# Kernel tuning notes

Measured on AMD Instinct MI355X. Metric: run time of the kernel, lower is better.

## Reference

```python
import jax, jax.numpy as jnp
import numpy as np

D_MODEL = 1024
NUM_HEADS = 16
DEPTH = D_MODEL // NUM_HEADS  # 64
BATCH = 2
SEQ = 2048


def setup_inputs() -> dict:
    key = jax.random.key(0)
    ks = jax.random.split(key, 11)
    s = 0.02
    return {
        "q": jax.random.normal(ks[0], (BATCH, SEQ, D_MODEL), dtype=jnp.float32),
        "k": jax.random.normal(ks[1], (BATCH, SEQ, D_MODEL), dtype=jnp.float32),
        "v": jax.random.normal(ks[2], (BATCH, SEQ, D_MODEL), dtype=jnp.float32),
        "wq": jax.random.normal(ks[3], (D_MODEL, D_MODEL), dtype=jnp.float32) * s,
        "bq": jnp.zeros((D_MODEL,), dtype=jnp.float32),
        "wk": jax.random.normal(ks[4], (D_MODEL, D_MODEL), dtype=jnp.float32) * s,
        "bk": jnp.zeros((D_MODEL,), dtype=jnp.float32),
        "wv": jax.random.normal(ks[5], (D_MODEL, D_MODEL), dtype=jnp.float32) * s,
        "bv": jnp.zeros((D_MODEL,), dtype=jnp.float32),
        "wo": jax.random.normal(ks[6], (D_MODEL, D_MODEL), dtype=jnp.float32) * s,
        "bo": jnp.zeros((D_MODEL,), dtype=jnp.float32),
    }


def reference(q, k, v, wq, bq, wk, bk, wv, bv, wo, bo):
    B = q.shape[0]
    # QKV projections, then split heads: (B, S, H, D)
    qh = (q @ wq + bq).reshape(B, -1, NUM_HEADS, DEPTH)
    kh = (k @ wk + bk).reshape(B, -1, NUM_HEADS, DEPTH)
    vh = (v @ wv + bv).reshape(B, -1, NUM_HEADS, DEPTH)

    inv_sqrt_dk = 1.0 / jnp.sqrt(jnp.float32(DEPTH))
    # scores: (B, Lq, Lk, H)
    scores = jnp.einsum('blhd,bjhd->bljh', qh, kh) * inv_sqrt_dk
    attn = jax.nn.softmax(scores, axis=2)
    # NOTE: original code divides by sqrt(dk) a SECOND time after softmax (faithful quirk)
    attn = attn * inv_sqrt_dk
    out = jnp.einsum('bljh,bjhe->blhe', attn, vh).reshape(B, -1, NUM_HEADS * DEPTH)
    return out @ wo + bo
```

## Files before the change

### kernel.cpp

```cpp
#include <hip/hip_runtime.h>
#include <math.h>

#define D_MODEL 1024
#define NHEADS 16
#define DH 64
#define BATCH 2
#define SEQ 2048
#define M_TOTAL (BATCH * SEQ)

typedef __attribute__((ext_vector_type(8))) short bf16x8;
typedef __attribute__((ext_vector_type(4))) float f32x4;
typedef __attribute__((ext_vector_type(16))) float f32x16;
typedef __attribute__((ext_vector_type(8))) unsigned short ushort8;
typedef unsigned short u16;
typedef unsigned int u32;

#define SCALE_Q 0.18033688f

static __device__ __forceinline__ u16 f2bf(float x) {
  unsigned int u = __float_as_uint(x);
  unsigned int r = (u + 0x7fffu + ((u >> 16) & 1u)) >> 16;
  return (u16)r;
}
static __device__ __forceinline__ u32 pk2bf(float a, float b) {
  return (u32)f2bf(a) | ((u32)f2bf(b) << 16);
}
static __device__ __forceinline__ u32 pkhu(float a, float b) {
  u32 ua = __float_as_uint(a) + 0x8000u;
  u32 ub = __float_as_uint(b) + 0x8000u;
  return (ua >> 16) | (ub & 0xffff0000u);
}
static __device__ __forceinline__ float exp2fast(float x) {
  return __builtin_amdgcn_exp2f(x);
}

static __device__ __forceinline__ void gl_lds16(const u16* g, u16* l) {
  __builtin_amdgcn_global_load_lds(
      (const __attribute__((address_space(1))) u32*)g,
      (__attribute__((address_space(3))) u32*)l, 16, 0, 0);
}

__global__ __launch_bounds__(256) void cvt_kernel(
    const float* __restrict__ q, const float* __restrict__ k, const float* __restrict__ v,
    u16* __restrict__ qb, u16* __restrict__ kb, u16* __restrict__ vb) {
  const int z = blockIdx.z;
  const float* src = (z == 0) ? q : (z == 1) ? k : v;
  u16* dst = (z == 0) ? qb : (z == 1) ? kb : vb;
  const size_t i = ((size_t)blockIdx.x * 256 + threadIdx.x) * 8;
  float4 a = *reinterpret_cast<const float4*>(src + i);
  float4 b = *reinterpret_cast<const float4*>(src + i + 4);
  u32 o0 = pk2bf(a.x, a.y), o1 = pk2bf(a.z, a.w);
  u32 o2 = pk2bf(b.x, b.y), o3 = pk2bf(b.z, b.w);
  *reinterpret_cast<uint4*>(dst + i) = make_uint4(o0, o1, o2, o3);
}

__global__ __launch_bounds__(256) void wtrans_kernel(
    const float* __restrict__ w0, const float* __restrict__ w1,
    const float* __restrict__ w2, const float* __restrict__ w3,
    u16* __restrict__ t0, u16* __restrict__ t1,
    u16* __restrict__ t2, u16* __restrict__ t3) {
  __shared__ float tf[64 * 68];
  const int z = blockIdx.z;
  const float* w = (z == 0) ? w0 : (z == 1) ? w1 : (z == 2) ? w2 : w3;
  u16* wt = (z == 0) ? t0 : (z == 1) ? t1 : (z == 2) ? t2 : t3;
  const int n0 = blockIdx.x * 64, k0 = blockIdx.y * 64;
  const int tid = threadIdx.x;
  const int kl = tid >> 4, nq = (tid & 15) * 4;
#pragma unroll
  for (int c = 0; c < 4; ++c) {
    float4 v = *reinterpret_cast<const float4*>(
        &w[(size_t)(k0 + kl + c * 16) * 1024 + n0 + nq]);
    *reinterpret_cast<float4*>(&tf[(kl + c * 16) * 68 + nq]) = v;
  }
  __syncthreads();
  const int n = tid & 63, kq = tid >> 6;
  u32 pk[8];
#pragma unroll
  for (int p = 0; p < 8; ++p) {
    float a = tf[(kq * 16 + 2 * p) * 68 + n];
    float b = tf[(kq * 16 + 2 * p + 1) * 68 + n];
    pk[p] = pk2bf(a, b);
  }
  u16* dst = &wt[(size_t)(n0 + n) * 1024 + k0 + kq * 16];
  *reinterpret_cast<uint4*>(dst) = make_uint4(pk[0], pk[1], pk[2], pk[3]);
  *reinterpret_cast<uint4*>(dst + 8) = make_uint4(pk[4], pk[5], pk[6], pk[7]);
}

__global__ __launch_bounds__(256) void qkv_gemm_kernel(
    const u16* __restrict__ qb, const u16* __restrict__ kb, const u16* __restrict__ vb,
    const u16* __restrict__ wqT, const u16* __restrict__ wkT, const u16* __restrict__ wvT,
    const float* __restrict__ bq, const float* __restrict__ bk, const float* __restrict__ bv,
    u16* __restrict__ qh, u16* __restrict__ kh, u16* __restrict__ vhT) {
  __shared__ u16 lds[9216];
  u16* sA = lds;
  u16* sB = lds + 4096;

  const int z = blockIdx.z;
  const u16* A  = (z == 0) ? qb : (z == 1) ? kb : vb;
  const u16* BT = (z == 0) ? wqT : (z == 1) ? wkT : wvT;
  const float* bias = (z == 0) ? bq : (z == 1) ? bk : bv;

  int wg = blockIdx.x + 8 * blockIdx.y;
  wg = (wg & 7) * 32 + (wg >> 3);
  const int m0 = (wg >> 3) * 128;
  const int n0 = (wg & 7) * 128;

  const int tid = threadIdx.x;
  const int w = tid >> 6, l = tid & 63;
  const int wr = w >> 1, wc = w & 1;
  const int n = l & 15, g = l >> 4;

  const u16* Ab = A + (size_t)(m0 + w * 16 + (l >> 2)) * 1024 + (l & 3) * 8;
  const u16* Bb = BT + (size_t)(n0 + w * 16 + (l >> 2)) * 1024 + (l & 3) * 8;
  u16* sAb = sA + w * 512;
  u16* sBb = sB + w * 512;

  f32x4 acc[4][4];
#pragma unroll
  for (int fm = 0; fm < 4; ++fm)
#pragma unroll
    for (int fn = 0; fn < 4; ++fn) acc[fm][fn] = (f32x4)(0.0f);

  for (int kk = 0; kk < 1024; kk += 32) {
    __syncthreads();
    gl_lds16(Ab + kk, sAb);
    gl_lds16(Ab + kk + (size_t)64 * 1024, sAb + 2048);
    gl_lds16(Bb + kk, sBb);
    gl_lds16(Bb + kk + (size_t)64 * 1024, sBb + 2048);
    __syncthreads();
    bf16x8 af[4], bf[4];
#pragma unroll
    for (int f = 0; f < 4; ++f)
      af[f] = *reinterpret_cast<const bf16x8*>(&sA[(wr * 64 + f * 16 + n) * 32 + g * 8]);
#pragma unroll
    for (int f = 0; f < 4; ++f)
      bf[f] = *reinterpret_cast<const bf16x8*>(&sB[(wc * 64 + f * 16 + n) * 32 + g * 8]);
#pragma unroll
    for (int fm = 0; fm < 4; ++fm)
#pragma unroll
      for (int fn = 0; fn < 4; ++fn)
        acc[fm][fn] = __builtin_amdgcn_mfma_f32_16x16x32_bf16(af[fm], bf[fn], acc[fm][fn], 0, 0, 0);
  }

  float bv4[4];
#pragma unroll
  for (int fn = 0; fn < 4; ++fn) bv4[fn] = bias[n0 + wc * 64 + fn * 16 + n];

  if (z < 2) {
    const float scale = (z == 0) ? SCALE_Q : 1.0f;
    u16* dst = (z == 0) ? qh : kh;
#pragma unroll
    for (int fm = 0; fm < 4; ++fm)
#pragma unroll
      for (int fn = 0; fn < 4; ++fn)
#pragma unroll
        for (int rr = 0; rr < 4; ++rr) {
          const int row = m0 + wr * 64 + fm * 16 + g * 4 + rr;
          const int col = n0 + wc * 64 + fn * 16 + n;
          dst[(size_t)row * 1024 + col] = f2bf((acc[fm][fn][rr] + bv4[fn]) * scale);
        }
  } else {
    __syncthreads();
    u16* bw = lds + w * 2304;
    const int hh = (n0 >> 6) + wc;
    const int bb = m0 >> 11;
    const int c = l >> 1, half = l & 1;
    const int sbase = (m0 & 2047) + wr * 64 + half * 32;
#pragma unroll
    for (int p = 0; p < 2; ++p) {
#pragma unroll
      for (int fh = 0; fh < 2; ++fh) {
        const int fn = p * 2 + fh;
#pragma unroll
        for (int fm = 0; fm < 4; ++fm)
#pragma unroll
          for (int rr = 0; rr < 4; ++rr)
            bw[(fh * 16 + n) * 72 + fm * 16 + g * 4 + rr] =
                f2bf(acc[fm][fn][rr] + bv4[fn]);
      }
      __syncthreads();
      u16* gd = vhT + ((size_t)((bb * NHEADS + hh) * DH + p * 32 + c)) * SEQ + sbase;
#pragma unroll
      for (int j = 0; j < 4; ++j)
        *reinterpret_cast<uint4*>(gd + j * 8) =
            *reinterpret_cast<const uint4*>(&bw[c * 72 + half * 32 + j * 8]);
      __syncthreads();
    }
  }
}

__global__ __launch_bounds__(256) void out_gemm_kernel(
    const u16* __restrict__ aob, const u16* __restrict__ woT,
    const float* __restrict__ bo, float* __restrict__ out) {
  __shared__ u16 lds[6144];
  u16* sA = lds;
  u16* sB = lds + 4096;

  int wg = blockIdx.x + 16 * blockIdx.y;
  wg = (wg & 7) * 64 + (wg >> 3);
  const int m0 = (wg >> 4) * 128;
  const int n0 = (wg & 15) * 64;

  const int tid = threadIdx.x;
  const int w = tid >> 6, l = tid & 63;
  const int wr = w >> 1, wc = w & 1;
  const int n = l & 15, g = l >> 4;

  const u16* Ab = aob + (size_t)(m0 + w * 16 + (l >> 2)) * 1024 + (l & 3) * 8;
  const u16* Bb = woT + (size_t)(n0 + w * 16 + (l >> 2)) * 1024 + (l & 3) * 8;
  u16* sAb = sA + w * 512;
  u16* sBb = sB + w * 512;

  f32x4 acc[4][2];
#pragma unroll
  for (int fm = 0; fm < 4; ++fm)
#pragma unroll
    for (int fn = 0; fn < 2; ++fn) acc[fm][fn] = (f32x4)(0.0f);

  for (int kk = 0; kk < 1024; kk += 32) {
    __syncthreads();
    gl_lds16(Ab + kk, sAb);
    gl_lds16(Ab + kk + (size_t)64 * 1024, sAb + 2048);
    gl_lds16(Bb + kk, sBb);
    __syncthreads();
    bf16x8 af[4], bf[2];
#pragma unroll
    for (int f = 0; f < 4; ++f)
      af[f] = *reinterpret_cast<const bf16x8*>(&sA[(wr * 64 + f * 16 + n) * 32 + g * 8]);
#pragma unroll
    for (int f = 0; f < 2; ++f)
      bf[f] = *reinterpret_cast<const bf16x8*>(&sB[(wc * 32 + f * 16 + n) * 32 + g * 8]);
#pragma unroll
    for (int fm = 0; fm < 4; ++fm)
#pragma unroll
      for (int fn = 0; fn < 2; ++fn)
        acc[fm][fn] = __builtin_amdgcn_mfma_f32_16x16x32_bf16(af[fm], bf[fn], acc[fm][fn], 0, 0, 0);
  }

  const float b0 = bo[n0 + wc * 32 + n];
  const float b1 = bo[n0 + wc * 32 + 16 + n];
#pragma unroll
  for (int fm = 0; fm < 4; ++fm)
#pragma unroll
    for (int rr = 0; rr < 4; ++rr) {
      const int row = m0 + wr * 64 + fm * 16 + g * 4 + rr;
      out[(size_t)row * 1024 + n0 + wc * 32 + n] = acc[fm][0][rr] + b0;
      out[(size_t)row * 1024 + n0 + wc * 32 + 16 + n] = acc[fm][1][rr] + b1;
    }
}

#define KT 64
__global__ __launch_bounds__(256, 2) void attn_mfma_kernel(
    const u16* __restrict__ qh, const u16* __restrict__ kh,
    const u16* __restrict__ vhT, u16* __restrict__ aob) {
  const int bid = blockIdx.x;
  const int xcd = bid & 7;
  const int idx = bid >> 3;
  const int bh = (xcd << 2) | (idx >> 4);
  const int qt = idx & 15;
  const int b = bh >> 4, h = bh & 15;

  const int tid = threadIdx.x;
  const int w = tid >> 6, l = tid & 63;
  const int lr = l & 31;
  const int g1 = l >> 5;
  const int q0 = qt * 128 + w * 32;

  __shared__ u16 Ks[2][KT * DH];
  __shared__ u16 Vs[2][DH * KT];
  __shared__ float Ls[4][32];

  bf16x8 qf[4];
#pragma unroll
  for (int kq = 0; kq < 4; ++kq)
    qf[kq] = *reinterpret_cast<const bf16x8*>(
        &qh[((size_t)(b * SEQ + q0 + lr)) * D_MODEL + h * DH + kq * 16 + g1 * 8]);

  f32x16 O0 = (f32x16)(0.0f), O1 = (f32x16)(0.0f);
  float lsum = 0.0f;

  const int srow = tid >> 2, sq = tid & 3;
  const u16* kp0 = kh + (size_t)(b * SEQ + srow) * D_MODEL + h * DH + sq * 16;
  const u16* vp0 = vhT + ((size_t)((b * NHEADS + h) * DH + srow)) * SEQ + sq * 16;
  const int sbase = srow * 64 + sq * 16;
  const int sxor = (srow & 7) << 3;
  const int rxor = (lr & 7) << 3;

  ushort8 kr[2], vr[2];
#pragma unroll
  for (int c = 0; c < 2; ++c) {
    kr[c] = *reinterpret_cast<const ushort8*>(kp0 + c * 8);
    vr[c] = *reinterpret_cast<const ushort8*>(vp0 + c * 8);
  }
#pragma unroll
  for (int c = 0; c < 2; ++c) {
    const int sidx = (sbase + c * 8) ^ sxor;
    *reinterpret_cast<ushort8*>(&Ks[0][sidx]) = kr[c];
    *reinterpret_cast<ushort8*>(&Vs[0][sidx]) = vr[c];
  }
  __syncthreads();

  int cur = 0;
  for (int jt = 0; jt < SEQ / KT; ++jt) {
    if (jt + 1 < SEQ / KT) {
      const int off = (jt + 1) * KT;
#pragma unroll
      for (int c = 0; c < 2; ++c) {
        kr[c] = *reinterpret_cast<const ushort8*>(kp0 + (size_t)off * D_MODEL + c * 8);
        vr[c] = *reinterpret_cast<const ushort8*>(vp0 + off + c * 8);
      }
    }

    __builtin_amdgcn_s_setprio(1);
    f32x16 St0 = (f32x16)(0.0f), St1 = (f32x16)(0.0f);
#pragma unroll
    for (int kq = 0; kq < 4; ++kq) {
      const int coff = kq * 16 + g1 * 8;
      bf16x8 kf0 = *reinterpret_cast<const bf16x8*>(&Ks[cur][(lr * 64 + coff) ^ rxor]);
      bf16x8 kf1 = *reinterpret_cast<const bf16x8*>(&Ks[cur][((32 + lr) * 64 + coff) ^ rxor]);
      St0 = __builtin_amdgcn_mfma_f32_32x32x16_bf16(kf0, qf[kq], St0, 0, 0, 0);
      St1 = __builtin_amdgcn_mfma_f32_32x32x16_bf16(kf1, qf[kq], St1, 0, 0, 0);
    }
    __builtin_amdgcn_s_setprio(0);

    u32 U0[8], U1[8];
#pragma unroll
    for (int s = 0; s < 8; ++s) {
      float a0 = exp2fast(St0[2 * s]), b0 = exp2fast(St0[2 * s + 1]);
      float a1 = exp2fast(St1[2 * s]), b1 = exp2fast(St1[2 * s + 1]);
      lsum += (a0 + b0) + (a1 + b1);
      U0[s] = pkhu(a0, b0);
      U1[s] = pkhu(a1, b1);
    }

    __builtin_amdgcn_s_setprio(1);
#pragma unroll
    for (int kb2 = 0; kb2 < 2; ++kb2) {
#pragma unroll
      for (int m16 = 0; m16 < 2; ++m16) {
        union { u32 u[4]; bf16x8 v; } pa;
        if (kb2 == 0) {
          pa.u[0] = U0[m16 * 4 + 0]; pa.u[1] = U0[m16 * 4 + 1];
          pa.u[2] = U0[m16 * 4 + 2]; pa.u[3] = U0[m16 * 4 + 3];
        } else {
          pa.u[0] = U1[m16 * 4 + 0]; pa.u[1] = U1[m16 * 4 + 1];
          pa.u[2] = U1[m16 * 4 + 2]; pa.u[3] = U1[m16 * 4 + 3];
        }
        const int koff = kb2 * 32 + m16 * 16 + g1 * 4;
        union { u32 u[4]; bf16x8 v; } vb0, vb1;
        *reinterpret_cast<uint2*>(&vb0.u[0]) =
            *reinterpret_cast<const uint2*>(&Vs[cur][(lr * 64 + koff) ^ rxor]);
        *reinterpret_cast<uint2*>(&vb0.u[2]) =
            *reinterpret_cast<const uint2*>(&Vs[cur][(lr * 64 + koff + 8) ^ rxor]);
        *reinterpret_cast<uint2*>(&vb1.u[0]) =
            *reinterpret_cast<const uint2*>(&Vs[cur][((32 + lr) * 64 + koff) ^ rxor]);
        *reinterpret_cast<uint2*>(&vb1.u[2]) =
            *reinterpret_cast<const uint2*>(&Vs[cur][((32 + lr) * 64 + koff + 8) ^ rxor]);
        O0 = __builtin_amdgcn_mfma_f32_32x32x16_bf16(pa.v, vb0.v, O0, 0, 0, 0);
        O1 = __builtin_amdgcn_mfma_f32_32x32x16_bf16(pa.v, vb1.v, O1, 0, 0, 0);
      }
    }
    __builtin_amdgcn_s_setprio(0);

    if (jt + 1 < SEQ / KT) {
#pragma unroll
      for (int c = 0; c < 2; ++c) {
        const int sidx = (sbase + c * 8) ^ sxor;
        *reinterpret_cast<ushort8*>(&Ks[cur ^ 1][sidx]) = kr[c];
        *reinterpret_cast<ushort8*>(&Vs[cur ^ 1][sidx]) = vr[c];
      }
    }
    __syncthreads();
    cur ^= 1;
  }

  lsum += (float)__shfl_xor(lsum, 32);
  if (g1 == 0) Ls[w][lr] = lsum;
  float invr[16];
#pragma unroll
  for (int c = 0; c < 4; ++c) {
    float4 lv = *reinterpret_cast<const float4*>(&Ls[w][c * 8 + g1 * 4]);
    invr[c * 4 + 0] = 0.125f / lv.x;
    invr[c * 4 + 1] = 0.125f / lv.y;
    invr[c * 4 + 2] = 0.125f / lv.z;
    invr[c * 4 + 3] = 0.125f / lv.w;
  }
#pragma unroll
  for (int dblk = 0; dblk < 2; ++dblk) {
#pragma unroll
    for (int s = 0; s < 8; ++s) {
      const int r0 = 2 * s, r1 = 2 * s + 1;
      float x0 = (dblk ? O1[r0] : O0[r0]) * invr[r0];
      float x1 = (dblk ? O1[r1] : O0[r1]) * invr[r1];
      const int row0 = q0 + (r0 & 3) + 8 * (r0 >> 2) + 4 * g1;
      const int row1 = q0 + (r1 & 3) + 8 * (r1 >> 2) + 4 * g1;
      const int col = h * DH + dblk * 32 + lr;
      aob[((size_t)(b * SEQ + row0)) * D_MODEL + col] = f2bf(x0);
      aob[((size_t)(b * SEQ + row1)) * D_MODEL + col] = f2bf(x1);
    }
  }
}

extern "C" void kernel_launch(void* const* d_in, const int* in_sizes, int n_in,
                              void* d_out, int out_size, void* d_ws, size_t ws_size,
                              hipStream_t stream) {
  const float* q  = (const float*)d_in[0];
  const float* k  = (const float*)d_in[1];
  const float* v  = (const float*)d_in[2];
  const float* wq = (const float*)d_in[3];
  const float* bq = (const float*)d_in[4];
  const float* wk = (const float*)d_in[5];
  const float* bk = (const float*)d_in[6];
  const float* wv = (const float*)d_in[7];
  const float* bv = (const float*)d_in[8];
  const float* wo = (const float*)d_in[9];
  const float* bo = (const float*)d_in[10];
  float* out = (float*)d_out;

  const size_t wcount = (size_t)D_MODEL * D_MODEL;
  const size_t tcount = (size_t)M_TOTAL * D_MODEL;
  u16* wqT = (u16*)d_ws;
  u16* wkT = wqT + wcount;
  u16* wvT = wkT + wcount;
  u16* woT = wvT + wcount;
  u16* qb  = woT + wcount;
  u16* kb  = qb + tcount;
  u16* vb  = kb + tcount;
  u16* qh  = vb + tcount;
  u16* kh  = qh + tcount;
  u16* vhT = kh + tcount;
  u16* aob = qb;

  dim3 blk(256);

  cvt_kernel<<<dim3(2048, 1, 3), blk, 0, stream>>>(q, k, v, qb, kb, vb);
  wtrans_kernel<<<dim3(16, 16, 4), blk, 0, stream>>>(wq, wk, wv, wo, wqT, wkT, wvT, woT);

  qkv_gemm_kernel<<<dim3(8, 32, 3), blk, 0, stream>>>(
      qb, kb, vb, wqT, wkT, wvT, bq, bk, bv, qh, kh, vhT);

  attn_mfma_kernel<<<dim3(512), dim3(256), 0, stream>>>(qh, kh, vhT, aob);

  out_gemm_kernel<<<dim3(16, 32), blk, 0, stream>>>(aob, woT, bo, out);
}
```

Before: 136.7 us.

## Split attention KV range across wave pairs with smaller query tiles

The attention kernel now processes 64-query tiles per block across 1024 blocks instead of 128-query tiles across 512. Pairs of waves split the key sequence in halves (a split-K over keys) with 32-key tiles, and the partial outputs and row sums are combined through shared memory at the end. V tiles use a padded layout instead of the XOR swizzle. The aim is more blocks and occupancy (launch bounds raised to 4) and shorter per-wave loops, at the cost of a final reduction through shared memory and more K/V reloading per query.

```diff
diff --git a/kernel.cpp b/kernel.cpp
--- a/kernel.cpp
+++ b/kernel.cpp
@@ -249,26 +249,28 @@
     }
 }
 
-#define KT 64
-__global__ __launch_bounds__(256, 2) void attn_mfma_kernel(
+#define KT2 32
+__global__ __launch_bounds__(256, 4) void attn_mfma_kernel(
     const u16* __restrict__ qh, const u16* __restrict__ kh,
     const u16* __restrict__ vhT, u16* __restrict__ aob) {
   const int bid = blockIdx.x;
   const int xcd = bid & 7;
   const int idx = bid >> 3;
-  const int bh = (xcd << 2) | (idx >> 4);
-  const int qt = idx & 15;
+  const int bh = (xcd << 2) | (idx >> 5);
+  const int qt = idx & 31;
   const int b = bh >> 4, h = bh & 15;
 
   const int tid = threadIdx.x;
   const int w = tid >> 6, l = tid & 63;
-  const int lr = l & 31;
-  const int g1 = l >> 5;
-  const int q0 = qt * 128 + w * 32;
-
-  __shared__ u16 Ks[2][KT * DH];
-  __shared__ u16 Vs[2][DH * KT];
+  const int qsub = w & 1;
+  const int khalf = w >> 1;
+  const int lr = l & 31, g1 = l >> 5;
+  const int q0 = qt * 64 + qsub * 32;
+
+  __shared__ u16 Ks[2][2][KT2 * DH];
+  __shared__ u16 Vs[2][2][DH * 40];
   __shared__ float Ls[4][32];
+  float* Cbuf = (float*)&Ks[0][0][0];
 
   bf16x8 qf[4];
 #pragma unroll
@@ -279,11 +281,15 @@
   f32x16 O0 = (f32x16)(0.0f), O1 = (f32x16)(0.0f);
   float lsum = 0.0f;
 
-  const int srow = tid >> 2, sq = tid & 3;
-  const u16* kp0 = kh + (size_t)(b * SEQ + srow) * D_MODEL + h * DH + sq * 16;
-  const u16* vp0 = vhT + ((size_t)((b * NHEADS + h) * DH + srow)) * SEQ + sq * 16;
-  const int sbase = srow * 64 + sq * 16;
-  const int sxor = (srow & 7) << 3;
+  const int stid = tid & 127;
+  const int sw = tid >> 7;
+  const int srow = stid >> 2, sq = stid & 3;
+  const int svrow = stid >> 1, svq = (stid & 1) * 16;
+  const u16* kp0 = kh + (size_t)(b * SEQ + sw * 1024 + srow) * D_MODEL + h * DH + sq * 16;
+  const u16* vp0 = vhT + ((size_t)((b * NHEADS + h) * DH + svrow)) * SEQ + sw * 1024 + svq;
+  const int ksbase = srow * 64 + sq * 16;
+  const int ksxor = (srow & 7) << 3;
+  const int vsbase = svrow * 40 + svq;
   const int rxor = (lr & 7) << 3;
 
   ushort8 kr[2], vr[2];
@@ -294,16 +300,16 @@
   }
 #pragma unroll
   for (int c = 0; c < 2; ++c) {
-    const int sidx = (sbase + c * 8) ^ sxor;
-    *reinterpret_cast<ushort8*>(&Ks[0][sidx]) = kr[c];
-    *reinterpret_cast<ushort8*>(&Vs[0][sidx]) = vr[c];
+    *reinterpret_cast<ushort8*>(&Ks[sw][0][(ksbase + c * 8) ^ ksxor]) = kr[c];
+    *reinterpret_cast<ushort8*>(&Vs[sw][0][vsbase + c * 8]) = vr[c];
   }
   __syncthreads();
 
   int cur = 0;
-  for (int jt = 0; jt < SEQ / KT; ++jt) {
-    if (jt + 1 < SEQ / KT) {
-      const int off = (jt + 1) * KT;
+  const int NT = 1024 / KT2;
+  for (int jt = 0; jt < NT; ++jt) {
+    if (jt + 1 < NT) {
+      const int off = (jt + 1) * KT2;
 #pragma unroll
       for (int c = 0; c < 2; ++c) {
         kr[c] = *reinterpret_cast<const ushort8*>(kp0 + (size_t)off * D_MODEL + c * 8);
@@ -312,91 +318,95 @@
     }
 
     __builtin_amdgcn_s_setprio(1);
-    f32x16 St0 = (f32x16)(0.0f), St1 = (f32x16)(0.0f);
+    f32x16 St0 = (f32x16)(0.0f);
 #pragma unroll
     for (int kq = 0; kq < 4; ++kq) {
       const int coff = kq * 16 + g1 * 8;
-      bf16x8 kf0 = *reinterpret_cast<const bf16x8*>(&Ks[cur][(lr * 64 + coff) ^ rxor]);
-      bf16x8 kf1 = *reinterpret_cast<const bf16x8*>(&Ks[cur][((32 + lr) * 64 + coff) ^ rxor]);
-      St0 = __builtin_amdgcn_mfma_f32_32x32x16_bf16(kf0, qf[kq], St0, 0, 0, 0);
-      St1 = __builtin_amdgcn_mfma_f32_32x32x16_bf16(kf1, qf[kq], St1, 0, 0, 0);
+      bf16x8 kf = *reinterpret_cast<const bf16x8*>(&Ks[khalf][cur][(lr * 64 + coff) ^ rxor]);
+      St0 = __builtin_amdgcn_mfma_f32_32x32x16_bf16(kf, qf[kq], St0, 0, 0, 0);
     }
     __builtin_amdgcn_s_setprio(0);
 
-    u32 U0[8], U1[8];
+    u32 U0[8];
 #pragma unroll
     for (int s = 0; s < 8; ++s) {
       float a0 = exp2fast(St0[2 * s]), b0 = exp2fast(St0[2 * s + 1]);
-      float a1 = exp2fast(St1[2 * s]), b1 = exp2fast(St1[2 * s + 1]);
-      lsum += (a0 + b0) + (a1 + b1);
+      lsum += a0 + b0;
       U0[s] = pkhu(a0, b0);
-      U1[s] = pkhu(a1, b1);
     }
 
     __builtin_amdgcn_s_setprio(1);
 #pragma unroll
-    for (int kb2 = 0; kb2 < 2; ++kb2) {
-#pragma unroll
-      for (int m16 = 0; m16 < 2; ++m16) {
-        union { u32 u[4]; bf16x8 v; } pa;
-        if (kb2 == 0) {
-          pa.u[0] = U0[m16 * 4 + 0]; pa.u[1] = U0[m16 * 4 + 1];
-          pa.u[2] = U0[m16 * 4 + 2]; pa.u[3] = U0[m16 * 4 + 3];
-        } else {
-          pa.u[0] = U1[m16 * 4 + 0]; pa.u[1] = U1[m16 * 4 + 1];
-          pa.u[2] = U1[m16 * 4 + 2]; pa.u[3] = U1[m16 * 4 + 3];
-        }
-        const int koff = kb2 * 32 + m16 * 16 + g1 * 4;
-        union { u32 u[4]; bf16x8 v; } vb0, vb1;
-        *reinterpret_cast<uint2*>(&vb0.u[0]) =
-            *reinterpret_cast<const uint2*>(&Vs[cur][(lr * 64 + koff) ^ rxor]);
-        *reinterpret_cast<uint2*>(&vb0.u[2]) =
-            *reinterpret_cast<const uint2*>(&Vs[cur][(lr * 64 + koff + 8) ^ rxor]);
-        *reinterpret_cast<uint2*>(&vb1.u[0]) =
-            *reinterpret_cast<const uint2*>(&Vs[cur][((32 + lr) * 64 + koff) ^ rxor]);
-        *reinterpret_cast<uint2*>(&vb1.u[2]) =
-            *reinterpret_cast<const uint2*>(&Vs[cur][((32 + lr) * 64 + koff + 8) ^ rxor]);
-        O0 = __builtin_amdgcn_mfma_f32_32x32x16_bf16(pa.v, vb0.v, O0, 0, 0, 0);
-        O1 = __builtin_amdgcn_mfma_f32_32x32x16_bf16(pa.v, vb1.v, O1, 0, 0, 0);
+    for (int m16 = 0; m16 < 2; ++m16) {
+      union { u32 u[4]; bf16x8 v; } pa;
+      pa.u[0] = U0[m16 * 4 + 0]; pa.u[1] = U0[m16 * 4 + 1];
+      pa.u[2] = U0[m16 * 4 + 2]; pa.u[3] = U0[m16 * 4 + 3];
+      const int koff = m16 * 16 + g1 * 4;
+      union { u32 u[4]; bf16x8 v; } vb0, vb1;
+      *reinterpret_cast<uint2*>(&vb0.u[0]) =
+          *reinterpret_cast<const uint2*>(&Vs[khalf][cur][lr * 40 + koff]);
+      *reinterpret_cast<uint2*>(&vb0.u[2]) =
+          *reinterpret_cast<const uint2*>(&Vs[khalf][cur][lr * 40 + koff + 8]);
+      *reinterpret_cast<uint2*>(&vb1.u[0]) =
+          *reinterpret_cast<const uint2*>(&Vs[khalf][cur][(32 + lr) * 40 + koff]);
+      *reinterpret_cast<uint2*>(&vb1.u[2]) =
+          *reinterpret_cast<const uint2*>(&Vs[khalf][cur][(32 + lr) * 40 + koff + 8]);
+      O0 = __builtin_amdgcn_mfma_f32_32x32x16_bf16(pa.v, vb0.v, O0, 0, 0, 0);
+      O1 = __builtin_amdgcn_mfma_f32_32x32x16_bf16(pa.v, vb1.v, O1, 0, 0, 0);
+    }
+    __builtin_amdgcn_s_setprio(0);
+
+    if (jt + 1 < NT) {
+#pragma unroll
+      for (int c = 0; c < 2; ++c) {
+        *reinterpret_cast<ushort8*>(&Ks[sw][cur ^ 1][(ksbase + c * 8) ^ ksxor]) = kr[c];
+        *reinterpret_cast<ushort8*>(&Vs[sw][cur ^ 1][vsbase + c * 8]) = vr[c];
       }
     }
-    __builtin_amdgcn_s_setprio(0);
-
-    if (jt + 1 < SEQ / KT) {
-#pragma unroll
-      for (int c = 0; c < 2; ++c) {
-        const int sidx = (sbase + c * 8) ^ sxor;
-        *reinterpret_cast<ushort8*>(&Ks[cur ^ 1][sidx]) = kr[c];
-        *reinterpret_cast<ushort8*>(&Vs[cur ^ 1][sidx]) = vr[c];
+    __syncthreads();
+    cur ^= 1;
+  }
+
+  lsum += (float)__shfl_xor(lsum, 32);
+  __syncthreads();
+  if (khalf == 1) {
+    if (g1 == 0) Ls[2 + qsub][lr] = lsum;
+#pragma unroll
+    for (int r = 0; r < 16; ++r) Cbuf[(qsub * 32 + r) * 64 + l] = O0[r];
+#pragma unroll
+    for (int r = 0; r < 16; ++r) Cbuf[(qsub * 32 + 16 + r) * 64 + l] = O1[r];
+  }
+  __syncthreads();
+  if (khalf == 0) {
+#pragma unroll
+    for (int r = 0; r < 16; ++r) O0[r] += Cbuf[(qsub * 32 + r) * 64 + l];
+#pragma unroll
+    for (int r = 0; r < 16; ++r) O1[r] += Cbuf[(qsub * 32 + 16 + r) * 64 + l];
+    const float ltot = lsum + Ls[2 + qsub][lr];
+    if (g1 == 0) Ls[qsub][lr] = ltot;
+
+    float invr[16];
+#pragma unroll
+    for (int c = 0; c < 4; ++c) {
+      float4 lv = *reinterpret_cast<const float4*>(&Ls[qsub][c * 8 + g1 * 4]);
+      invr[c * 4 + 0] = 0.125f / lv.x;
+      invr[c * 4 + 1] = 0.125f / lv.y;
+      invr[c * 4 + 2] = 0.125f / lv.z;
+      invr[c * 4 + 3] = 0.125f / lv.w;
+    }
+#pragma unroll
+    for (int dblk = 0; dblk < 2; ++dblk) {
+#pragma unroll
+      for (int s = 0; s < 8; ++s) {
+        const int r0 = 2 * s, r1 = 2 * s + 1;
+        float x0 = (dblk ? O1[r0] : O0[r0]) * invr[r0];
+        float x1 = (dblk ? O1[r1] : O0[r1]) * invr[r1];
+        const int row0 = q0 + (r0 & 3) + 8 * (r0 >> 2) + 4 * g1;
+        const int row1 = q0 + (r1 & 3) + 8 * (r1 >> 2) + 4 * g1;
+        const int col = h * DH + dblk * 32 + lr;
+        aob[((size_t)(b * SEQ + row0)) * D_MODEL + col] = f2bf(x0);
+        aob[((size_t)(b * SEQ + row1)) * D_MODEL + col] = f2bf(x1);
       }
-    }
-    __syncthreads();
-    cur ^= 1;
-  }
-
-  lsum += (float)__shfl_xor(lsum, 32);
-  if (g1 == 0) Ls[w][lr] = lsum;
-  float invr[16];
-#pragma unroll
-  for (int c = 0; c < 4; ++c) {
-    float4 lv = *reinterpret_cast<const float4*>(&Ls[w][c * 8 + g1 * 4]);
-    invr[c * 4 + 0] = 0.125f / lv.x;
-    invr[c * 4 + 1] = 0.125f / lv.y;
-    invr[c * 4 + 2] = 0.125f / lv.z;
-    invr[c * 4 + 3] = 0.125f / lv.w;
-  }
-#pragma unroll
-  for (int dblk = 0; dblk < 2; ++dblk) {
-#pragma unroll
-    for (int s = 0; s < 8; ++s) {
-      const int r0 = 2 * s, r1 = 2 * s + 1;
-      float x0 = (dblk ? O1[r0] : O0[r0]) * invr[r0];
-      float x1 = (dblk ? O1[r1] : O0[r1]) * invr[r1];
-      const int row0 = q0 + (r0 & 3) + 8 * (r0 >> 2) + 4 * g1;
-      const int row1 = q0 + (r1 & 3) + 8 * (r1 >> 2) + 4 * g1;
-      const int col = h * DH + dblk * 32 + lr;
-      aob[((size_t)(b * SEQ + row0)) * D_MODEL + col] = f2bf(x0);
-      aob[((size_t)(b * SEQ + row1)) * D_MODEL + col] = f2bf(x1);
     }
   }
 }
@@ -439,7 +449,7 @@
   qkv_gemm_kernel<<<dim3(8, 32, 3), blk, 0, stream>>>(
       qb, kb, vb, wqT, wkT, wvT, bq, bk, bv, qh, kh, vhT);
 
-  attn_mfma_kernel<<<dim3(512), dim3(256), 0, stream>>>(qh, kh, vhT, aob);
+  attn_mfma_kernel<<<dim3(1024), blk, 0, stream>>>(qh, kh, vhT, aob);
 
   out_gemm_kernel<<<dim3(16, 32), blk, 0, stream>>>(aob, woT, bo, out);
 }
```

Result: slower. 141.6 us (+3.6%).
